# Performance work log

Measured on AMD Instinct MI355X. Metric: run time of the kernel, lower is better.

Reference implementation:

```python
import jax, jax.numpy as jnp
import numpy as np

NUM_STREAM = 4
SINKHORN_ITERS = 20
HC_EPS = 1e-06
NORM_EPS = 1e-06


def sinkhorn_knopps(h, iters, eps):
    # h: [B, S, ns, ns]
    h = jax.nn.softmax(h, axis=-1) + eps
    h = h / (h.sum(-2, keepdims=True) + eps)
    for _ in range(iters - 1):  # fixed small trip count (19), unrolled
        h = h / (h.sum(-1, keepdims=True) + eps)
        h = h / (h.sum(-2, keepdims=True) + eps)
    return h


def setup_inputs() -> dict:
    key = jax.random.key(0)
    k1, k2, k3, k4 = jax.random.split(key, 4)
    B, S, ns, H = 4, 2048, NUM_STREAM, 1024
    mix_hc = (2 + ns) * ns  # 24
    x = jax.random.normal(k1, (B, S, ns, H), dtype=jnp.float32)
    hc_fn = jax.random.normal(k2, (mix_hc, ns * H), dtype=jnp.float32) * 0.02
    hc_scale = jax.random.uniform(k3, (3,), dtype=jnp.float32)
    hc_base = jax.random.normal(k4, (mix_hc,), dtype=jnp.float32)
    return {"x": x, "hc_fn": hc_fn, "hc_scale": hc_scale, "hc_base": hc_base}


def reference(x, hc_fn, hc_scale, hc_base):
    B, S, ns, H = x.shape
    xf = x.reshape(B, S, ns * H).astype(jnp.float32)
    # RMSNorm stats (applied as a post-scale on the linear output, as in source)
    rsqrt = jax.lax.rsqrt(jnp.mean(jnp.square(xf), axis=-1, keepdims=True) + NORM_EPS)
    weight = jnp.einsum('bsd,md->bsm', xf, hc_fn) * rsqrt  # [B, S, mix_hc]
    h_pre = weight[..., :ns]
    h_post = weight[..., ns:2 * ns]
    h_res = weight[..., 2 * ns:].reshape(B, S, ns, ns)
    h_pre = jax.nn.sigmoid(h_pre * hc_scale[0] + hc_base[:ns][None, None, :]) + HC_EPS
    h_post = 2.0 * jax.nn.sigmoid(h_post * hc_scale[1] + hc_base[ns:2 * ns][None, None, :])
    h_res = h_res * hc_scale[2] + hc_base[2 * ns:].reshape(ns, ns)[None, None, :, :]
    h_res = sinkhorn_knopps(h_res, SINKHORN_ITERS, HC_EPS)
    xs = xf.reshape(B, S, ns, H)
    # hc_pre: mix streams into a single vector per token
    y = jnp.einsum('bsn,bsnh->bsh', h_pre, xs)  # [B, S, H]
    # hc_post: broadcast gated y back to streams + Sinkhorn-mixed residual streams
    out = h_post[..., None] * y[:, :, None, :] + jnp.einsum('bsij,bsih->bsjh', h_res, xs)
    return out.astype(x.dtype)
```

## Files before the change

kernel.cpp:

```cpp
#include <hip/hip_runtime.h>
#include <math.h>

#define NS 4
#define HDIM 1024
#define DDIM 4096
#define TOK_B 16
#define KCH 512
#define NPS 32
#define HC_EPS_F 1e-6f
#define NORM_EPS_F 1e-6f

typedef __attribute__((ext_vector_type(8))) short short8;
typedef __attribute__((ext_vector_type(4))) float f32x4;

__device__ __forceinline__ float frcp(float v) { return __builtin_amdgcn_rcpf(v); }

__device__ __forceinline__ void gload_lds16(const float* g, float* l) {
  __builtin_amdgcn_global_load_lds(
      (const __attribute__((address_space(1))) void*)g,
      (__attribute__((address_space(3))) void*)l, 16, 0, 0);
}

#define CVT_PAIR(j, f0, f1)                                                     \
  { unsigned p0 = __float_as_uint(f0), p1 = __float_as_uint(f1);                \
    H.u[j] = (p1 & 0xFFFF0000u) | (p0 >> 16);                                   \
    unsigned q0 = __float_as_uint((f0) - __uint_as_float(p0 & 0xFFFF0000u));    \
    unsigned q1 = __float_as_uint((f1) - __uint_as_float(p1 & 0xFFFF0000u));    \
    L.u[j] = (q1 & 0xFFFF0000u) | (q0 >> 16); }

__device__ __forceinline__ void cvt_hl(const float4 a, const float4 b,
                                       short8& hi, short8& lo) {
  union { unsigned u[4]; short8 s; } H, L;
  CVT_PAIR(0, a.x, a.y)
  CVT_PAIR(1, a.z, a.w)
  CVT_PAIR(2, b.x, b.y)
  CVT_PAIR(3, b.z, b.w)
  hi = H.s; lo = L.s;
}

__launch_bounds__(256, 4)
__global__ void mhc_convb(const float* __restrict__ hc_fn,
                          unsigned short* __restrict__ bh,
                          unsigned short* __restrict__ bl) {
  const int g = blockIdx.x * 256 + threadIdx.x;
  const float4 v = ((const float4*)hc_fn)[g];
  ushort4 h, l;
  unsigned p;
  p = __float_as_uint(v.x); h.x = p >> 16; l.x = __float_as_uint(v.x - __uint_as_float(p & 0xFFFF0000u)) >> 16;
  p = __float_as_uint(v.y); h.y = p >> 16; l.y = __float_as_uint(v.y - __uint_as_float(p & 0xFFFF0000u)) >> 16;
  p = __float_as_uint(v.z); h.z = p >> 16; l.z = __float_as_uint(v.z - __uint_as_float(p & 0xFFFF0000u)) >> 16;
  p = __float_as_uint(v.w); h.w = p >> 16; l.w = __float_as_uint(v.w - __uint_as_float(p & 0xFFFF0000u)) >> 16;
  ((ushort4*)bh)[g] = h;
  ((ushort4*)bl)[g] = l;
}

__launch_bounds__(256, 2)
__global__ void mhc_dots_mfma(const float* __restrict__ x,
                              const unsigned short* __restrict__ bh,
                              const unsigned short* __restrict__ bl,
                              float* __restrict__ wp, int ntok) {
  __shared__ float xs[TOK_B * KCH];
  const int tid  = threadIdx.x;
  const int lane = tid & 63;
  const int wave = tid >> 6;
  const int mt = blockIdx.x >> 3;
  const int kc = blockIdx.x & 7;
  const long long tok0 = (long long)mt * TOK_B;
  const int k0 = kc * KCH;

  #pragma unroll
  for (int c = 0; c < 8; ++c) {
    const int S = c * 256 + wave * 64;
    const int t = S >> 7;
    const int c4src = (((wave & 1) * 64 + lane) ^ (t & 7));
    gload_lds16(x + (tok0 + t) * DDIM + k0 + c4src * 4, xs + (size_t)S * 4);
  }

  const int kh  = wave;
  const int row = lane & 15;
  const int ks  = lane >> 4;

  const unsigned short* bp0h = bh + (long long)row * DDIM + k0 + kh * 128 + ks * 8;
  const unsigned short* bp0l = bl + (long long)row * DDIM + k0 + kh * 128 + ks * 8;
  const int fr1c = (row < 8) ? (16 + row) : 23;
  const unsigned short* bp1h = bh + (long long)fr1c * DDIM + k0 + kh * 128 + ks * 8;
  const unsigned short* bp1l = bl + (long long)fr1c * DDIM + k0 + kh * 128 + ks * 8;
  const bool v1 = (row < 8);
  const short8 z8 = {0, 0, 0, 0, 0, 0, 0, 0};

  f32x4 acc0 = {0.f, 0.f, 0.f, 0.f};
  f32x4 acc1 = {0.f, 0.f, 0.f, 0.f};
  float ssq = 0.f;

  short8 b0h_c = *(const short8*)bp0h;
  short8 b0l_c = *(const short8*)bp0l;
  short8 b1h_c = v1 ? *(const short8*)bp1h : z8;
  short8 b1l_c = v1 ? *(const short8*)bp1l : z8;

  __syncthreads();

  const int rsw = row & 7;
  const float* arow = xs + (size_t)row * KCH;

  #pragma unroll
  for (int s = 0; s < 4; ++s) {
    short8 b0h_n, b0l_n, b1h_n, b1l_n;
    if (s < 3) {
      const int o = (s + 1) * 32;
      b0h_n = *(const short8*)(bp0h + o);
      b0l_n = *(const short8*)(bp0l + o);
      b1h_n = v1 ? *(const short8*)(bp1h + o) : z8;
      b1l_n = v1 ? *(const short8*)(bp1l + o) : z8;
    }
    const int c4 = kh * 32 + s * 8 + ks * 2;
    const float4 a0 = *(const float4*)(arow + (size_t)(c4 ^ rsw) * 4);
    const float4 a1 = *(const float4*)(arow + (size_t)((c4 + 1) ^ rsw) * 4);

    ssq = fmaf(a0.x, a0.x, fmaf(a0.y, a0.y, fmaf(a0.z, a0.z, fmaf(a0.w, a0.w, ssq))));
    ssq = fmaf(a1.x, a1.x, fmaf(a1.y, a1.y, fmaf(a1.z, a1.z, fmaf(a1.w, a1.w, ssq))));

    short8 ahi, alo;
    cvt_hl(a0, a1, ahi, alo);

    acc0 = __builtin_amdgcn_mfma_f32_16x16x32_bf16(ahi, b0h_c, acc0, 0, 0, 0);
    acc1 = __builtin_amdgcn_mfma_f32_16x16x32_bf16(ahi, b1h_c, acc1, 0, 0, 0);
    acc0 = __builtin_amdgcn_mfma_f32_16x16x32_bf16(ahi, b0l_c, acc0, 0, 0, 0);
    acc1 = __builtin_amdgcn_mfma_f32_16x16x32_bf16(ahi, b1l_c, acc1, 0, 0, 0);
    acc0 = __builtin_amdgcn_mfma_f32_16x16x32_bf16(alo, b0h_c, acc0, 0, 0, 0);
    acc1 = __builtin_amdgcn_mfma_f32_16x16x32_bf16(alo, b1h_c, acc1, 0, 0, 0);

    if (s < 3) {
      b0h_c = b0h_n; b0l_c = b0l_n;
      b1h_c = b1h_n; b1l_c = b1l_n;
    }
  }

  ssq += __shfl_xor(ssq, 16, 64);
  ssq += __shfl_xor(ssq, 32, 64);

  const int ps = kc * 4 + kh;
  float* wpk = wp + (long long)ps * ntok * 25;
  if (lane < 16) wpk[(tok0 + lane) * 25 + 24] = ssq;
  const int rq = lane >> 4;
  #pragma unroll
  for (int r = 0; r < 4; ++r)
    wpk[(tok0 + rq * 4 + r) * 25 + row] = acc0[r];
  if (row < 8) {
    #pragma unroll
    for (int r = 0; r < 4; ++r)
      wpk[(tok0 + rq * 4 + r) * 25 + 16 + row] = acc1[r];
  }
}

__launch_bounds__(256, 4)
__global__ void mhc_sinkhorn(const float* __restrict__ wp,
                             const float* __restrict__ hc_scale,
                             const float* __restrict__ hc_base,
                             float* __restrict__ gates, int ntok) {
  const int lane = threadIdx.x & 63;
  const int wave = threadIdx.x >> 6;
  const long long tok = (long long)blockIdx.x * 16 + wave * 4 + (lane >> 4);
  const int e = lane & 15;

  const long long kstride = (long long)ntok * 25;
  const float* b = wp + tok * 25;
  float sres = 0.f, ssq = 0.f, spre = 0.f, spost = 0.f;
  #pragma unroll 4
  for (int ps = 0; ps < NPS; ++ps) {
    const float* p = b + ps * kstride;
    sres += p[8 + e];
    ssq  += p[24];
    if (e < NS) { spre += p[e]; spost += p[NS + e]; }
  }

  const float rs = rsqrtf(ssq * (1.0f / DDIM) + NORM_EPS_F);
  const float s0 = hc_scale[0], s1 = hc_scale[1], s2 = hc_scale[2];

  float h = sres * rs * s2 + hc_base[8 + e];
  float mx = fmaxf(h, __shfl_xor(h, 1, 4));
  mx = fmaxf(mx, __shfl_xor(mx, 2, 4));
  float ex = expf(h - mx);
  float sm = ex + __shfl_xor(ex, 1, 4);
  sm += __shfl_xor(sm, 2, 4);
  h = ex * frcp(sm) + HC_EPS_F;
  float cs = h + __shfl_xor(h, 4, 16);
  cs += __shfl_xor(cs, 8, 16);
  h *= frcp(cs + HC_EPS_F);
  #pragma unroll 1
  for (int itn = 0; itn < 19; ++itn) {
    float rsum = h + __shfl_xor(h, 1, 4);
    rsum += __shfl_xor(rsum, 2, 4);
    h *= frcp(rsum + HC_EPS_F);
    float csum = h + __shfl_xor(h, 4, 16);
    csum += __shfl_xor(csum, 8, 16);
    h *= frcp(csum + HC_EPS_F);
  }
  float* g = gates + tok * 24;
  g[8 + e] = h;
  if (e < NS) {
    g[e] = frcp(1.0f + expf(-(spre * rs * s0 + hc_base[e]))) + HC_EPS_F;
    g[NS + e] = 2.0f * frcp(1.0f + expf(-(spost * rs * s1 + hc_base[NS + e])));
  }
}

__launch_bounds__(256, 8)
__global__ void mhc_out(const float* __restrict__ x,
                        const float* __restrict__ gates,
                        float* __restrict__ out) {
  const long long token = blockIdx.x;
  const int q = threadIdx.x;

  const float* g = gates + token * 24;
  float hp[NS], hq[NS], hr[NS][NS];
  #pragma unroll
  for (int i = 0; i < NS; ++i) {
    hp[i] = g[i];
    hq[i] = g[NS + i];
    #pragma unroll
    for (int j = 0; j < NS; ++j) hr[i][j] = g[8 + i * NS + j];
  }

  const float4* xb = (const float4*)(x + token * DDIM);
  float4 xv[NS];
  #pragma unroll
  for (int i = 0; i < NS; ++i) xv[i] = xb[i * 256 + q];

  float4 y;
  y.x = hp[0]*xv[0].x + hp[1]*xv[1].x + hp[2]*xv[2].x + hp[3]*xv[3].x;
  y.y = hp[0]*xv[0].y + hp[1]*xv[1].y + hp[2]*xv[2].y + hp[3]*xv[3].y;
  y.z = hp[0]*xv[0].z + hp[1]*xv[1].z + hp[2]*xv[2].z + hp[3]*xv[3].z;
  y.w = hp[0]*xv[0].w + hp[1]*xv[1].w + hp[2]*xv[2].w + hp[3]*xv[3].w;

  float4* ob = (float4*)(out + token * DDIM);
  #pragma unroll
  for (int n = 0; n < NS; ++n) {
    float4 o;
    o.x = hq[n]*y.x + hr[0][n]*xv[0].x + hr[1][n]*xv[1].x + hr[2][n]*xv[2].x + hr[3][n]*xv[3].x;
    o.y = hq[n]*y.y + hr[0][n]*xv[0].y + hr[1][n]*xv[1].y + hr[2][n]*xv[2].y + hr[3][n]*xv[3].y;
    o.z = hq[n]*y.z + hr[0][n]*xv[0].z + hr[1][n]*xv[1].z + hr[2][n]*xv[2].z + hr[3][n]*xv[3].z;
    o.w = hq[n]*y.w + hr[0][n]*xv[0].w + hr[1][n]*xv[1].w + hr[2][n]*xv[2].w + hr[3][n]*xv[3].w;
    ob[n * 256 + q] = o;
  }
}

extern "C" void kernel_launch(void* const* d_in, const int* in_sizes, int n_in,
                              void* d_out, int out_size, void* d_ws, size_t ws_size,
                              hipStream_t stream) {
  const float* x        = (const float*)d_in[0];
  const float* hc_fn    = (const float*)d_in[1];
  const float* hc_scale = (const float*)d_in[2];
  const float* hc_base  = (const float*)d_in[3];
  float* out = (float*)d_out;

  const int ntok = in_sizes[0] / DDIM;
  float* gates = (float*)d_ws;

  float* wp = out;
  unsigned short* bh = (unsigned short*)(out + (size_t)NPS * ntok * 25);
  unsigned short* bl = bh + 24 * DDIM;

  mhc_convb<<<(24 * DDIM / 4) / 256, 256, 0, stream>>>(hc_fn, bh, bl);
  mhc_dots_mfma<<<(ntok / TOK_B) * 8, 256, 0, stream>>>(x, bh, bl, wp, ntok);
  mhc_sinkhorn<<<ntok / 16, 256, 0, stream>>>(wp, hc_scale, hc_base, gates, ntok);
  mhc_out<<<ntok, 256, 0, stream>>>(x, gates, out);
}
```

Measured before the change: 100.2 us.

## Replace split-K grid with in-block K loop and double-buffered LDS staging

The dot-product kernel no longer splits K across 8 blocks per 16-token tile. Each block now walks all 16 K-chunks of 256 floats, prefetching the next chunk into a second LDS buffer while it computes on the current one. The per-token partial-sum slices drop from 32 to 4, which cuts the partial-sum write traffic and the reads in the Sinkhorn reduction. In exchange the grid shrinks to 512 blocks, which lowers occupancy and latency hiding. The B-operand loads are no longer software-prefetched inside the loop.

After: 96.88 us. 3.3% less time.

```diff
diff --git a/kernel.cpp b/kernel.cpp
--- a/kernel.cpp
+++ b/kernel.cpp
@@ -5,8 +5,9 @@
 #define HDIM 1024
 #define DDIM 4096
 #define TOK_B 16
-#define KCH 512
-#define NPS 32
+#define KCH 256
+#define NCH 16
+#define NPS 4
 #define HC_EPS_F 1e-6f
 #define NORM_EPS_F 1e-6f
 
@@ -59,32 +60,44 @@
                               const unsigned short* __restrict__ bh,
                               const unsigned short* __restrict__ bl,
                               float* __restrict__ wp, int ntok) {
-  __shared__ float xs[TOK_B * KCH];
+  __shared__ float xs[2][TOK_B * KCH];
   const int tid  = threadIdx.x;
   const int lane = tid & 63;
   const int wave = tid >> 6;
-  const int mt = blockIdx.x >> 3;
-  const int kc = blockIdx.x & 7;
-  const long long tok0 = (long long)mt * TOK_B;
-  const int k0 = kc * KCH;
-
-  #pragma unroll
-  for (int c = 0; c < 8; ++c) {
-    const int S = c * 256 + wave * 64;
-    const int t = S >> 7;
-    const int c4src = (((wave & 1) * 64 + lane) ^ (t & 7));
-    gload_lds16(x + (tok0 + t) * DDIM + k0 + c4src * 4, xs + (size_t)S * 4);
+  const long long tok0 = (long long)blockIdx.x * TOK_B;
+
+#define STAGE(d, kcn)                                                           \
+  {                                                                             \
+    _Pragma("unroll")                                                           \
+    for (int c = 0; c < 4; ++c) {                                               \
+      const int t = c * 4 + wave;                                               \
+      const int c4src = lane ^ (t & 7);                                         \
+      gload_lds16(x + (tok0 + t) * DDIM + (kcn) * KCH + c4src * 4,              \
+                  &xs[d][(c * 4 + wave) * KCH + lane * 4 - lane * 4 + (c * 256 + wave * 64) * 4]); \
+    }                                                                           \
+  }
+#undef STAGE
+#define STAGE(d, kcn)                                                           \
+  {                                                                             \
+    _Pragma("unroll")                                                           \
+    for (int c = 0; c < 4; ++c) {                                               \
+      const int S = c * 256 + wave * 64;                  \
+      const int t = S >> 6;                                      \
+      const int c4src = lane ^ (t & 7);                                         \
+      gload_lds16(x + (tok0 + t) * DDIM + (kcn) * KCH + c4src * 4,              \
+                  &xs[d][(size_t)S * 4]);                                       \
+    }                                                                           \
   }
 
   const int kh  = wave;
   const int row = lane & 15;
   const int ks  = lane >> 4;
 
-  const unsigned short* bp0h = bh + (long long)row * DDIM + k0 + kh * 128 + ks * 8;
-  const unsigned short* bp0l = bl + (long long)row * DDIM + k0 + kh * 128 + ks * 8;
+  const unsigned short* bp0h = bh + (long long)row * DDIM + kh * 64 + ks * 8;
+  const unsigned short* bp0l = bl + (long long)row * DDIM + kh * 64 + ks * 8;
   const int fr1c = (row < 8) ? (16 + row) : 23;
-  const unsigned short* bp1h = bh + (long long)fr1c * DDIM + k0 + kh * 128 + ks * 8;
-  const unsigned short* bp1l = bl + (long long)fr1c * DDIM + k0 + kh * 128 + ks * 8;
+  const unsigned short* bp1h = bh + (long long)fr1c * DDIM + kh * 64 + ks * 8;
+  const unsigned short* bp1l = bl + (long long)fr1c * DDIM + kh * 64 + ks * 8;
   const bool v1 = (row < 8);
   const short8 z8 = {0, 0, 0, 0, 0, 0, 0, 0};
 
@@ -92,54 +105,52 @@
   f32x4 acc1 = {0.f, 0.f, 0.f, 0.f};
   float ssq = 0.f;
 
-  short8 b0h_c = *(const short8*)bp0h;
-  short8 b0l_c = *(const short8*)bp0l;
-  short8 b1h_c = v1 ? *(const short8*)bp1h : z8;
-  short8 b1l_c = v1 ? *(const short8*)bp1l : z8;
-
+  STAGE(0, 0)
   __syncthreads();
 
   const int rsw = row & 7;
-  const float* arow = xs + (size_t)row * KCH;
-
-  #pragma unroll
-  for (int s = 0; s < 4; ++s) {
-    short8 b0h_n, b0l_n, b1h_n, b1l_n;
-    if (s < 3) {
-      const int o = (s + 1) * 32;
-      b0h_n = *(const short8*)(bp0h + o);
-      b0l_n = *(const short8*)(bp0l + o);
-      b1h_n = v1 ? *(const short8*)(bp1h + o) : z8;
-      b1l_n = v1 ? *(const short8*)(bp1l + o) : z8;
+  const float* arow0 = xs[0] + (size_t)row * KCH;
+  const float* arow1 = xs[1] + (size_t)row * KCH;
+
+  for (int kc = 0; kc < NCH; ++kc) {
+    if (kc < NCH - 1) {
+      if (kc & 1) STAGE(0, kc + 1) else STAGE(1, kc + 1)
     }
-    const int c4 = kh * 32 + s * 8 + ks * 2;
-    const float4 a0 = *(const float4*)(arow + (size_t)(c4 ^ rsw) * 4);
-    const float4 a1 = *(const float4*)(arow + (size_t)((c4 + 1) ^ rsw) * 4);
-
-    ssq = fmaf(a0.x, a0.x, fmaf(a0.y, a0.y, fmaf(a0.z, a0.z, fmaf(a0.w, a0.w, ssq))));
-    ssq = fmaf(a1.x, a1.x, fmaf(a1.y, a1.y, fmaf(a1.z, a1.z, fmaf(a1.w, a1.w, ssq))));
-
-    short8 ahi, alo;
-    cvt_hl(a0, a1, ahi, alo);
-
-    acc0 = __builtin_amdgcn_mfma_f32_16x16x32_bf16(ahi, b0h_c, acc0, 0, 0, 0);
-    acc1 = __builtin_amdgcn_mfma_f32_16x16x32_bf16(ahi, b1h_c, acc1, 0, 0, 0);
-    acc0 = __builtin_amdgcn_mfma_f32_16x16x32_bf16(ahi, b0l_c, acc0, 0, 0, 0);
-    acc1 = __builtin_amdgcn_mfma_f32_16x16x32_bf16(ahi, b1l_c, acc1, 0, 0, 0);
-    acc0 = __builtin_amdgcn_mfma_f32_16x16x32_bf16(alo, b0h_c, acc0, 0, 0, 0);
-    acc1 = __builtin_amdgcn_mfma_f32_16x16x32_bf16(alo, b1h_c, acc1, 0, 0, 0);
-
-    if (s < 3) {
-      b0h_c = b0h_n; b0l_c = b0l_n;
-      b1h_c = b1h_n; b1l_c = b1l_n;
+    const float* arow = (kc & 1) ? arow1 : arow0;
+    const int kb = kc * KCH;
+
+    #pragma unroll
+    for (int s = 0; s < 2; ++s) {
+      const int ko = kb + s * 32;
+      const short8 b0h = *(const short8*)(bp0h + ko);
+      const short8 b0l = *(const short8*)(bp0l + ko);
+      const short8 b1h = v1 ? *(const short8*)(bp1h + ko) : z8;
+      const short8 b1l = v1 ? *(const short8*)(bp1l + ko) : z8;
+
+      const int c4 = kh * 16 + s * 8 + ks * 2;
+      const float4 a0 = *(const float4*)(arow + (size_t)(c4 ^ rsw) * 4);
+      const float4 a1 = *(const float4*)(arow + (size_t)((c4 + 1) ^ rsw) * 4);
+
+      ssq = fmaf(a0.x, a0.x, fmaf(a0.y, a0.y, fmaf(a0.z, a0.z, fmaf(a0.w, a0.w, ssq))));
+      ssq = fmaf(a1.x, a1.x, fmaf(a1.y, a1.y, fmaf(a1.z, a1.z, fmaf(a1.w, a1.w, ssq))));
+
+      short8 ahi, alo;
+      cvt_hl(a0, a1, ahi, alo);
+
+      acc0 = __builtin_amdgcn_mfma_f32_16x16x32_bf16(ahi, b0h, acc0, 0, 0, 0);
+      acc1 = __builtin_amdgcn_mfma_f32_16x16x32_bf16(ahi, b1h, acc1, 0, 0, 0);
+      acc0 = __builtin_amdgcn_mfma_f32_16x16x32_bf16(ahi, b0l, acc0, 0, 0, 0);
+      acc1 = __builtin_amdgcn_mfma_f32_16x16x32_bf16(ahi, b1l, acc1, 0, 0, 0);
+      acc0 = __builtin_amdgcn_mfma_f32_16x16x32_bf16(alo, b0h, acc0, 0, 0, 0);
+      acc1 = __builtin_amdgcn_mfma_f32_16x16x32_bf16(alo, b1h, acc1, 0, 0, 0);
     }
+    __syncthreads();
   }
 
   ssq += __shfl_xor(ssq, 16, 64);
   ssq += __shfl_xor(ssq, 32, 64);
 
-  const int ps = kc * 4 + kh;
-  float* wpk = wp + (long long)ps * ntok * 25;
+  float* wpk = wp + (long long)kh * ntok * 25;
   if (lane < 16) wpk[(tok0 + lane) * 25 + 24] = ssq;
   const int rq = lane >> 4;
   #pragma unroll
@@ -150,6 +161,7 @@
     for (int r = 0; r < 4; ++r)
       wpk[(tok0 + rq * 4 + r) * 25 + 16 + row] = acc1[r];
   }
+#undef STAGE
 }
 
 __launch_bounds__(256, 4)
@@ -165,7 +177,7 @@
   const long long kstride = (long long)ntok * 25;
   const float* b = wp + tok * 25;
   float sres = 0.f, ssq = 0.f, spre = 0.f, spost = 0.f;
-  #pragma unroll 4
+  #pragma unroll
   for (int ps = 0; ps < NPS; ++ps) {
     const float* p = b + ps * kstride;
     sres += p[8 + e];
@@ -260,7 +272,7 @@
   unsigned short* bl = bh + 24 * DDIM;
 
   mhc_convb<<<(24 * DDIM / 4) / 256, 256, 0, stream>>>(hc_fn, bh, bl);
-  mhc_dots_mfma<<<(ntok / TOK_B) * 8, 256, 0, stream>>>(x, bh, bl, wp, ntok);
+  mhc_dots_mfma<<<ntok / TOK_B, 256, 0, stream>>>(x, bh, bl, wp, ntok);
   mhc_sinkhorn<<<ntok / 16, 256, 0, stream>>>(wp, hc_scale, hc_base, gates, ntok);
   mhc_out<<<ntok, 256, 0, stream>>>(x, gates, out);
 }
```

## Load x directly into registers per wave, dropping LDS staging in dots kernel

Applied to the files above, without the earlier changes.

The dots kernel no longer stages a 16x512 x tile in LDS through global_load_lds with a block barrier. Each wave now independently owns a 16-token by 256-column unit and reads x straight from global memory into registers. Partial sums drop from 32 to 16 slices, and launch bounds go up to 3 blocks per CU. This removes the LDS traffic and __syncthreads, but loses the explicit prefetch of B fragments and relies on strided per-lane global loads of x.

New measurement: 101.3 us. About the same (+1.2%).

```diff
diff --git a/kernel.cpp b/kernel.cpp
--- a/kernel.cpp
+++ b/kernel.cpp
@@ -4,9 +4,9 @@
 #define NS 4
 #define HDIM 1024
 #define DDIM 4096
-#define TOK_B 16
-#define KCH 512
-#define NPS 32
+#define MT 16
+#define KCH 256
+#define NPS 16
 #define HC_EPS_F 1e-6f
 #define NORM_EPS_F 1e-6f
 
@@ -14,12 +14,6 @@
 typedef __attribute__((ext_vector_type(4))) float f32x4;
 
 __device__ __forceinline__ float frcp(float v) { return __builtin_amdgcn_rcpf(v); }
-
-__device__ __forceinline__ void gload_lds16(const float* g, float* l) {
-  __builtin_amdgcn_global_load_lds(
-      (const __attribute__((address_space(1))) void*)g,
-      (__attribute__((address_space(3))) void*)l, 16, 0, 0);
-}
 
 #define CVT_PAIR(j, f0, f1)                                                     \
   { unsigned p0 = __float_as_uint(f0), p1 = __float_as_uint(f1);                \
@@ -54,37 +48,28 @@
   ((ushort4*)bl)[g] = l;
 }
 
-__launch_bounds__(256, 2)
+__launch_bounds__(256, 3)
 __global__ void mhc_dots_mfma(const float* __restrict__ x,
                               const unsigned short* __restrict__ bh,
                               const unsigned short* __restrict__ bl,
                               float* __restrict__ wp, int ntok) {
-  __shared__ float xs[TOK_B * KCH];
-  const int tid  = threadIdx.x;
-  const int lane = tid & 63;
-  const int wave = tid >> 6;
-  const int mt = blockIdx.x >> 3;
-  const int kc = blockIdx.x & 7;
-  const long long tok0 = (long long)mt * TOK_B;
+  const int lane = threadIdx.x & 63;
+  const int wave = threadIdx.x >> 6;
+  const int unit = blockIdx.x * 4 + wave;
+  const int mt = unit >> 4;
+  const int kc = unit & 15;
+  const long long tok0 = (long long)mt * MT;
   const int k0 = kc * KCH;
 
-  #pragma unroll
-  for (int c = 0; c < 8; ++c) {
-    const int S = c * 256 + wave * 64;
-    const int t = S >> 7;
-    const int c4src = (((wave & 1) * 64 + lane) ^ (t & 7));
-    gload_lds16(x + (tok0 + t) * DDIM + k0 + c4src * 4, xs + (size_t)S * 4);
-  }
-
-  const int kh  = wave;
   const int row = lane & 15;
   const int ks  = lane >> 4;
 
-  const unsigned short* bp0h = bh + (long long)row * DDIM + k0 + kh * 128 + ks * 8;
-  const unsigned short* bp0l = bl + (long long)row * DDIM + k0 + kh * 128 + ks * 8;
+  const float4* ap = (const float4*)(x + (tok0 + row) * DDIM + k0) + ks * 2;
+  const unsigned short* bp0h = bh + (long long)row * DDIM + k0 + ks * 8;
+  const unsigned short* bp0l = bl + (long long)row * DDIM + k0 + ks * 8;
   const int fr1c = (row < 8) ? (16 + row) : 23;
-  const unsigned short* bp1h = bh + (long long)fr1c * DDIM + k0 + kh * 128 + ks * 8;
-  const unsigned short* bp1l = bl + (long long)fr1c * DDIM + k0 + kh * 128 + ks * 8;
+  const unsigned short* bp1h = bh + (long long)fr1c * DDIM + k0 + ks * 8;
+  const unsigned short* bp1l = bl + (long long)fr1c * DDIM + k0 + ks * 8;
   const bool v1 = (row < 8);
   const short8 z8 = {0, 0, 0, 0, 0, 0, 0, 0};
 
@@ -92,29 +77,14 @@
   f32x4 acc1 = {0.f, 0.f, 0.f, 0.f};
   float ssq = 0.f;
 
-  short8 b0h_c = *(const short8*)bp0h;
-  short8 b0l_c = *(const short8*)bp0l;
-  short8 b1h_c = v1 ? *(const short8*)bp1h : z8;
-  short8 b1l_c = v1 ? *(const short8*)bp1l : z8;
-
-  __syncthreads();
-
-  const int rsw = row & 7;
-  const float* arow = xs + (size_t)row * KCH;
-
-  #pragma unroll
-  for (int s = 0; s < 4; ++s) {
-    short8 b0h_n, b0l_n, b1h_n, b1l_n;
-    if (s < 3) {
-      const int o = (s + 1) * 32;
-      b0h_n = *(const short8*)(bp0h + o);
-      b0l_n = *(const short8*)(bp0l + o);
-      b1h_n = v1 ? *(const short8*)(bp1h + o) : z8;
-      b1l_n = v1 ? *(const short8*)(bp1l + o) : z8;
-    }
-    const int c4 = kh * 32 + s * 8 + ks * 2;
-    const float4 a0 = *(const float4*)(arow + (size_t)(c4 ^ rsw) * 4);
-    const float4 a1 = *(const float4*)(arow + (size_t)((c4 + 1) ^ rsw) * 4);
+  #pragma unroll
+  for (int s = 0; s < KCH / 32; ++s) {
+    const float4 a0 = ap[s * 8];
+    const float4 a1 = ap[s * 8 + 1];
+    const short8 b0h = *(const short8*)(bp0h + s * 32);
+    const short8 b0l = *(const short8*)(bp0l + s * 32);
+    const short8 b1h = v1 ? *(const short8*)(bp1h + s * 32) : z8;
+    const short8 b1l = v1 ? *(const short8*)(bp1l + s * 32) : z8;
 
     ssq = fmaf(a0.x, a0.x, fmaf(a0.y, a0.y, fmaf(a0.z, a0.z, fmaf(a0.w, a0.w, ssq))));
     ssq = fmaf(a1.x, a1.x, fmaf(a1.y, a1.y, fmaf(a1.z, a1.z, fmaf(a1.w, a1.w, ssq))));
@@ -122,24 +92,18 @@
     short8 ahi, alo;
     cvt_hl(a0, a1, ahi, alo);
 
-    acc0 = __builtin_amdgcn_mfma_f32_16x16x32_bf16(ahi, b0h_c, acc0, 0, 0, 0);
-    acc1 = __builtin_amdgcn_mfma_f32_16x16x32_bf16(ahi, b1h_c, acc1, 0, 0, 0);
-    acc0 = __builtin_amdgcn_mfma_f32_16x16x32_bf16(ahi, b0l_c, acc0, 0, 0, 0);
-    acc1 = __builtin_amdgcn_mfma_f32_16x16x32_bf16(ahi, b1l_c, acc1, 0, 0, 0);
-    acc0 = __builtin_amdgcn_mfma_f32_16x16x32_bf16(alo, b0h_c, acc0, 0, 0, 0);
-    acc1 = __builtin_amdgcn_mfma_f32_16x16x32_bf16(alo, b1h_c, acc1, 0, 0, 0);
-
-    if (s < 3) {
-      b0h_c = b0h_n; b0l_c = b0l_n;
-      b1h_c = b1h_n; b1l_c = b1l_n;
-    }
+    acc0 = __builtin_amdgcn_mfma_f32_16x16x32_bf16(ahi, b0h, acc0, 0, 0, 0);
+    acc1 = __builtin_amdgcn_mfma_f32_16x16x32_bf16(ahi, b1h, acc1, 0, 0, 0);
+    acc0 = __builtin_amdgcn_mfma_f32_16x16x32_bf16(ahi, b0l, acc0, 0, 0, 0);
+    acc1 = __builtin_amdgcn_mfma_f32_16x16x32_bf16(ahi, b1l, acc1, 0, 0, 0);
+    acc0 = __builtin_amdgcn_mfma_f32_16x16x32_bf16(alo, b0h, acc0, 0, 0, 0);
+    acc1 = __builtin_amdgcn_mfma_f32_16x16x32_bf16(alo, b1h, acc1, 0, 0, 0);
   }
 
   ssq += __shfl_xor(ssq, 16, 64);
   ssq += __shfl_xor(ssq, 32, 64);
 
-  const int ps = kc * 4 + kh;
-  float* wpk = wp + (long long)ps * ntok * 25;
+  float* wpk = wp + (long long)kc * ntok * 25;
   if (lane < 16) wpk[(tok0 + lane) * 25 + 24] = ssq;
   const int rq = lane >> 4;
   #pragma unroll
@@ -260,7 +224,8 @@
   unsigned short* bl = bh + 24 * DDIM;
 
   mhc_convb<<<(24 * DDIM / 4) / 256, 256, 0, stream>>>(hc_fn, bh, bl);
-  mhc_dots_mfma<<<(ntok / TOK_B) * 8, 256, 0, stream>>>(x, bh, bl, wp, ntok);
+  const int units = (ntok / MT) * NPS;
+  mhc_dots_mfma<<<units / 4, 256, 0, stream>>>(x, bh, bl, wp, ntok);
   mhc_sinkhorn<<<ntok / 16, 256, 0, stream>>>(wp, hc_scale, hc_base, gates, ntok);
   mhc_out<<<ntok, 256, 0, stream>>>(x, gates, out);
 }
```
